# Performance work log

Measured on AMD Instinct MI355X. Metric: run time of the kernel, lower is better.

The kernel has to match this reference:

```python
import jax, jax.numpy as jnp
import numpy as np

# SelectiveAttention (keras) reference.
# - A single shared InputDense (D -> key_dim) projects query, key, value.
# - ComponentBuilder yields (filter_input=Q, context_input=banded K^T, _input=V):
#   scores = (Q K^T / sqrt(key_dim)) masked to the band |i-j| <= band_size
#   (the layer's Softmax sublayer is built but never invoked in call()).
# - attended = scores @ V, then OutputDense (key_dim -> D). Dropout inactive at inference.

def setup_inputs() -> dict:
    key = jax.random.key(0)
    ks = jax.random.split(key, 5)
    B, S, D, Dk = 4, 4096, 512, 64
    query = jax.random.normal(ks[0], (B, S, D), dtype=jnp.float32)
    value = jax.random.normal(ks[1], (B, S, D), dtype=jnp.float32)
    Wi = jax.random.normal(ks[2], (D, Dk), dtype=jnp.float32) * (1.0 / np.sqrt(D))
    bi = jnp.zeros((Dk,), dtype=jnp.float32)
    Wo = jax.random.normal(ks[3], (Dk, D), dtype=jnp.float32) * (1.0 / np.sqrt(Dk))
    bo = jnp.zeros((D,), dtype=jnp.float32)
    return {"query": query, "value": value, "Wi": Wi, "bi": bi,
            "Wo": Wo, "bo": bo, "band_size": 128}


def reference(query, value, Wi, bi, Wo, bo, band_size):
    Dk = Wi.shape[1]
    scale = 1.0 / jnp.sqrt(jnp.asarray(Dk, dtype=query.dtype))
    # shared input projection (same dense for q, k, v; key defaults to value)
    q = query @ Wi + bi            # [B,S,Dk]
    kv = value @ Wi + bi           # [B,S,Dk]  (k == v here)
    scores = jnp.einsum('bqd,bkd->bqk', q, kv) * scale  # [B,S,S]
    S = q.shape[1]
    idx = jnp.arange(S)
    band = (jnp.abs(idx[:, None] - idx[None, :]) <= band_size)  # [S,S] bool
    scores = jnp.where(band[None], scores, 0.0)
    attended = jnp.einsum('bqk,bkd->bqd', scores, kv)    # [B,S,Dk]
    return attended @ Wo + bo                            # [B,S,D]
```

## Files before the change

### kernel.cpp

```cpp
#include <hip/hip_runtime.h>
#include <math.h>


typedef __bf16 bf16;
using bf16x4  = __attribute__((ext_vector_type(4))) __bf16;
using bf16x8  = __attribute__((ext_vector_type(8))) __bf16;
using floatx4 = __attribute__((ext_vector_type(4))) float;

#define MFMA(a, b, c) __builtin_amdgcn_mfma_f32_16x16x32_bf16(a, b, c, 0, 0, 0)

__global__ __launch_bounds__(256) void prep_weights(
    const float* __restrict__ Wi, const float* __restrict__ Wo,
    bf16* __restrict__ WiT, bf16* __restrict__ WoT)
{
    __shared__ float T[64][65];
    const int blk = blockIdx.x, tid = threadIdx.x;
    if (blk < 8) {
        const int k0 = blk * 64;
        #pragma unroll
        for (int i = 0; i < 4; i++) {
            int idx4 = tid * 4 + i;
            int r = idx4 >> 4, c4 = (idx4 & 15) * 4;
            float4 f = *(const float4*)(Wi + (size_t)(k0 + r) * 64 + c4);
            T[r][c4 + 0] = f.x; T[r][c4 + 1] = f.y;
            T[r][c4 + 2] = f.z; T[r][c4 + 3] = f.w;
        }
        __syncthreads();
        #pragma unroll
        for (int i = 0; i < 2; i++) {
            int seg = tid * 2 + i;
            int n = seg >> 3, k8 = (seg & 7) * 8;
            bf16x8 v;
            #pragma unroll
            for (int j = 0; j < 8; j++) v[j] = (bf16)T[k8 + j][n];
            *(bf16x8*)(WiT + (size_t)n * 512 + k0 + k8) = v;
        }
    } else {
        const int n0 = (blk - 8) * 64;
        #pragma unroll
        for (int i = 0; i < 4; i++) {
            int idx4 = tid * 4 + i;
            int r = idx4 >> 4, c4 = (idx4 & 15) * 4;
            float4 f = *(const float4*)(Wo + (size_t)r * 512 + n0 + c4);
            T[r][c4 + 0] = f.x; T[r][c4 + 1] = f.y;
            T[r][c4 + 2] = f.z; T[r][c4 + 3] = f.w;
        }
        __syncthreads();
        #pragma unroll
        for (int i = 0; i < 2; i++) {
            int seg = tid * 2 + i;
            int n = seg >> 3, k8 = (seg & 7) * 8;
            bf16x8 v;
            #pragma unroll
            for (int j = 0; j < 8; j++) v[j] = (bf16)T[k8 + j][n];
            *(bf16x8*)(WoT + (size_t)(n0 + n) * 64 + k8) = v;
        }
    }
}

__global__ __launch_bounds__(256) void proj_in_kernel(
    const float* __restrict__ q, const float* __restrict__ v,
    const bf16* __restrict__ WiT, const float* __restrict__ bi,
    bf16* __restrict__ qp, bf16* __restrict__ kvp, bf16* __restrict__ kvT,
    int K, int S)
{
    const float* x = blockIdx.z ? v : q;
    bf16* y = blockIdx.z ? kvp : qp;
    __shared__ float P[4][16][68];
    const int tid = threadIdx.x;
    const int wave = tid >> 6, lane = tid & 63;
    const int lr = lane & 15, lq = lane >> 4;
    const int row0 = blockIdx.x * 16;
    const float* xrow = x + (size_t)(row0 + lr) * K + wave * 128;
    const bf16* wrow = WiT + wave * 128;

    floatx4 acc[4] = {};
    #pragma unroll
    for (int ks = 0; ks < 4; ks++) {
        const int k0 = ks * 32 + lq * 8;
        float4 a0 = *(const float4*)(xrow + k0);
        float4 a1 = *(const float4*)(xrow + k0 + 4);
        bf16x8 af;
        af[0] = (bf16)a0.x; af[1] = (bf16)a0.y; af[2] = (bf16)a0.z; af[3] = (bf16)a0.w;
        af[4] = (bf16)a1.x; af[5] = (bf16)a1.y; af[6] = (bf16)a1.z; af[7] = (bf16)a1.w;
        #pragma unroll
        for (int t = 0; t < 4; t++) {
            bf16x8 bfv = *(const bf16x8*)(wrow + (size_t)(t * 16 + lr) * K + k0);
            acc[t] = MFMA(af, bfv, acc[t]);
        }
    }
    #pragma unroll
    for (int t = 0; t < 4; t++)
        #pragma unroll
        for (int r = 0; r < 4; r++)
            P[wave][lq * 4 + r][t * 16 + lr] = acc[t][r];
    __syncthreads();

    {
        const int row = tid >> 4, c4 = (tid & 15) * 4;
        float4 s0 = *(const float4*)&P[0][row][c4];
        float4 s1 = *(const float4*)&P[1][row][c4];
        float4 s2 = *(const float4*)&P[2][row][c4];
        float4 s3 = *(const float4*)&P[3][row][c4];
        float4 bb = *(const float4*)(bi + c4);
        bf16x4 o;
        o[0] = (bf16)(s0.x + s1.x + s2.x + s3.x + bb.x);
        o[1] = (bf16)(s0.y + s1.y + s2.y + s3.y + bb.y);
        o[2] = (bf16)(s0.z + s1.z + s2.z + s3.z + bb.z);
        o[3] = (bf16)(s0.w + s1.w + s2.w + s3.w + bb.w);
        *(bf16x4*)(y + (size_t)(row0 + row) * 64 + c4) = o;
    }
    if (blockIdx.z) {
        const int d = tid >> 2, s4 = (tid & 3) * 4;
        const int b = row0 >> 12, s0r = row0 & (S - 1);
        const float bb = bi[d];
        bf16x4 o;
        #pragma unroll
        for (int i = 0; i < 4; i++) {
            float s = P[0][s4 + i][d] + P[1][s4 + i][d]
                    + P[2][s4 + i][d] + P[3][s4 + i][d] + bb;
            o[i] = (bf16)s;
        }
        *(bf16x4*)(kvT + ((size_t)b * 64 + d) * S + s0r + s4) = o;
    }
}

__global__ __launch_bounds__(256) void band_attn_out_kernel(
    const bf16* __restrict__ qp, const bf16* __restrict__ kvp,
    const bf16* __restrict__ kvT, const int* __restrict__ band_ptr,
    const bf16* __restrict__ WoT, const float* __restrict__ bo,
    float* __restrict__ out, int S, float scale)
{
    __shared__ bf16 Ss[4][2][16][88];
    const int tid = threadIdx.x;
    const int wave = tid >> 6, lane = tid & 63;
    const int lr = lane & 15, lq = lane >> 4;
    const int gw = blockIdx.x * 4 + wave;
    const int b = gw >> 8;
    const int q0 = (gw & 255) * 16;
    const int band = band_ptr[0];

    const bf16* qb = qp + ((size_t)b * S + q0) * 64;
    bf16x8 qf0 = *(const bf16x8*)(qb + lr * 64 + lq * 8);
    bf16x8 qf1 = *(const bf16x8*)(qb + lr * 64 + 32 + lq * 8);

    floatx4 acc[4] = {};
    const int ch_lo = (q0 - band) >> 6;
    #pragma unroll
    for (int cc = 0; cc < 5; cc++) {
        const int kj0 = (ch_lo + cc) * 64;
        bf16 (*strip)[88] = Ss[wave][cc & 1];
        floatx4 sc[4] = {};
        #pragma unroll
        for (int t = 0; t < 4; t++) {
            int kr = kj0 + t * 16 + lr;
            int krc = min(max(kr, 0), S - 1);
            const bf16* kp = kvp + ((size_t)b * S + krc) * 64;
            bf16x8 b0 = *(const bf16x8*)(kp + lq * 8);
            bf16x8 b1 = *(const bf16x8*)(kp + 32 + lq * 8);
            sc[t] = MFMA(qf0, b0, sc[t]);
            sc[t] = MFMA(qf1, b1, sc[t]);
        }
        #pragma unroll
        for (int t = 0; t < 4; t++) {
            int kj = kj0 + t * 16 + lr;
            bool kv_ok = (kj >= 0) && (kj < S);
            #pragma unroll
            for (int r = 0; r < 4; r++) {
                int qi = q0 + lq * 4 + r;
                int dlt = qi - kj; dlt = dlt < 0 ? -dlt : dlt;
                float vv = (kv_ok && dlt <= band) ? sc[t][r] * scale : 0.f;
                strip[lq * 4 + r][t * 16 + lr] = (bf16)vv;
            }
        }
        #pragma unroll
        for (int ks = 0; ks < 2; ks++) {
            bf16x8 sa = *(const bf16x8*)(&strip[lr][ks * 32 + lq * 8]);
            int kb = kj0 + ks * 32 + lq * 8;
            int kbc = min(max(kb, 0), S - 8);
            #pragma unroll
            for (int t = 0; t < 4; t++) {
                bf16x8 vb = *(const bf16x8*)(kvT + ((size_t)b * 64 + t * 16 + lr) * S + kbc);
                acc[t] = MFMA(sa, vb, acc[t]);
            }
        }
    }

    bf16 (*strip)[88] = Ss[wave][0];
    #pragma unroll
    for (int t = 0; t < 4; t++)
        #pragma unroll
        for (int r = 0; r < 4; r++)
            strip[lq * 4 + r][t * 16 + lr] = (bf16)acc[t][r];
    bf16x8 af0 = *(const bf16x8*)(&strip[lr][lq * 8]);
    bf16x8 af1 = *(const bf16x8*)(&strip[lr][32 + lq * 8]);
    float* orow = out + ((size_t)b * S + q0) * 512;
    #pragma unroll 8
    for (int tp = 0; tp < 32; tp++) {
        const bf16* wp = WoT + (size_t)(tp * 16 + lr) * 64;
        bf16x8 b0 = *(const bf16x8*)(wp + lq * 8);
        bf16x8 b1 = *(const bf16x8*)(wp + 32 + lq * 8);
        floatx4 o = {};
        o = MFMA(af0, b0, o);
        o = MFMA(af1, b1, o);
        float bb = bo[tp * 16 + lr];
        #pragma unroll
        for (int r = 0; r < 4; r++)
            orow[(size_t)(lq * 4 + r) * 512 + tp * 16 + lr] = o[r] + bb;
    }
}

extern "C" void kernel_launch(void* const* d_in, const int* in_sizes, int n_in,
                              void* d_out, int out_size, void* d_ws, size_t ws_size,
                              hipStream_t stream) {
    const float* query = (const float*)d_in[0];
    const float* value = (const float*)d_in[1];
    const float* Wi    = (const float*)d_in[2];
    const float* bi    = (const float*)d_in[3];
    const float* Wo    = (const float*)d_in[4];
    const float* bo    = (const float*)d_in[5];
    const int*   band  = (const int*)d_in[6];
    float* out = (float*)d_out;

    const int Dk = in_sizes[3];
    const int D  = in_sizes[5];
    const int S  = 4096;
    const int BS = in_sizes[0] / D;
    const int B  = BS / S;
    const float scale = 1.0f / sqrtf((float)Dk);

    bf16* WiT = (bf16*)d_ws;
    bf16* WoT = WiT + 32768;
    bf16* qp  = WoT + 32768;
    bf16* kvp = qp  + (size_t)BS * 64;
    bf16* kvT = kvp + (size_t)BS * 64;

    prep_weights<<<16, 256, 0, stream>>>(Wi, Wo, WiT, WoT);

    proj_in_kernel<<<dim3(BS / 16, 1, 2), 256, 0, stream>>>(
        query, value, WiT, bi, qp, kvp, kvT, D, S);

    band_attn_out_kernel<<<dim3(BS / 64), 256, 0, stream>>>(
        qp, kvp, kvT, band, WoT, bo, out, S, scale);
}
```

Measured before the change: 150.9 us.

## Split band chunks and output projection across waves per query tile

Each block now handles a single 16-row query tile instead of four. Its waves split the five key chunks (wave 0 takes two) and reduce partial results through shared memory. The output projection is then split across waves, eight column tiles each. The softmax scale is folded into the Q projection so the attention loop skips a multiply. This launches four times more blocks to raise parallelism, at the cost of extra shared-memory reduction, two barriers and load imbalance across waves.

```diff
diff --git a/kernel.cpp b/kernel.cpp
--- a/kernel.cpp
+++ b/kernel.cpp
@@ -62,10 +62,11 @@
     const float* __restrict__ q, const float* __restrict__ v,
     const bf16* __restrict__ WiT, const float* __restrict__ bi,
     bf16* __restrict__ qp, bf16* __restrict__ kvp, bf16* __restrict__ kvT,
-    int K, int S)
+    int K, int S, float scale)
 {
     const float* x = blockIdx.z ? v : q;
     bf16* y = blockIdx.z ? kvp : qp;
+    const float sc = blockIdx.z ? 1.0f : scale;
     __shared__ float P[4][16][68];
     const int tid = threadIdx.x;
     const int wave = tid >> 6, lane = tid & 63;
@@ -104,10 +105,10 @@
         float4 s3 = *(const float4*)&P[3][row][c4];
         float4 bb = *(const float4*)(bi + c4);
         bf16x4 o;
-        o[0] = (bf16)(s0.x + s1.x + s2.x + s3.x + bb.x);
-        o[1] = (bf16)(s0.y + s1.y + s2.y + s3.y + bb.y);
-        o[2] = (bf16)(s0.z + s1.z + s2.z + s3.z + bb.z);
-        o[3] = (bf16)(s0.w + s1.w + s2.w + s3.w + bb.w);
+        o[0] = (bf16)((s0.x + s1.x + s2.x + s3.x + bb.x) * sc);
+        o[1] = (bf16)((s0.y + s1.y + s2.y + s3.y + bb.y) * sc);
+        o[2] = (bf16)((s0.z + s1.z + s2.z + s3.z + bb.z) * sc);
+        o[3] = (bf16)((s0.w + s1.w + s2.w + s3.w + bb.w) * sc);
         *(bf16x4*)(y + (size_t)(row0 + row) * 64 + c4) = o;
     }
     if (blockIdx.z) {
@@ -129,15 +130,17 @@
     const bf16* __restrict__ qp, const bf16* __restrict__ kvp,
     const bf16* __restrict__ kvT, const int* __restrict__ band_ptr,
     const bf16* __restrict__ WoT, const float* __restrict__ bo,
-    float* __restrict__ out, int S, float scale)
+    float* __restrict__ out, int S)
 {
-    __shared__ bf16 Ss[4][2][16][88];
+    __shared__ bf16 Ss[4][16][88];
+    __shared__ float P[4][16][68];
+    __shared__ bf16 St[16][72];
     const int tid = threadIdx.x;
     const int wave = tid >> 6, lane = tid & 63;
     const int lr = lane & 15, lq = lane >> 4;
-    const int gw = blockIdx.x * 4 + wave;
-    const int b = gw >> 8;
-    const int q0 = (gw & 255) * 16;
+    const int gs = blockIdx.x;
+    const int b = gs >> 8;
+    const int q0 = (gs & 255) * 16;
     const int band = band_ptr[0];
 
     const bf16* qb = qp + ((size_t)b * S + q0) * 64;
@@ -147,56 +150,74 @@
     floatx4 acc[4] = {};
     const int ch_lo = (q0 - band) >> 6;
     #pragma unroll
-    for (int cc = 0; cc < 5; cc++) {
-        const int kj0 = (ch_lo + cc) * 64;
-        bf16 (*strip)[88] = Ss[wave][cc & 1];
-        floatx4 sc[4] = {};
-        #pragma unroll
-        for (int t = 0; t < 4; t++) {
-            int kr = kj0 + t * 16 + lr;
-            int krc = min(max(kr, 0), S - 1);
-            const bf16* kp = kvp + ((size_t)b * S + krc) * 64;
-            bf16x8 b0 = *(const bf16x8*)(kp + lq * 8);
-            bf16x8 b1 = *(const bf16x8*)(kp + 32 + lq * 8);
-            sc[t] = MFMA(qf0, b0, sc[t]);
-            sc[t] = MFMA(qf1, b1, sc[t]);
-        }
-        #pragma unroll
-        for (int t = 0; t < 4; t++) {
-            int kj = kj0 + t * 16 + lr;
-            bool kv_ok = (kj >= 0) && (kj < S);
-            #pragma unroll
-            for (int r = 0; r < 4; r++) {
-                int qi = q0 + lq * 4 + r;
-                int dlt = qi - kj; dlt = dlt < 0 ? -dlt : dlt;
-                float vv = (kv_ok && dlt <= band) ? sc[t][r] * scale : 0.f;
-                strip[lq * 4 + r][t * 16 + lr] = (bf16)vv;
+    for (int pass = 0; pass < 2; pass++) {
+        const int cc = wave + pass * 4;
+        if (cc <= 4) {
+            const int kj0 = (ch_lo + cc) * 64;
+            floatx4 sc[4] = {};
+            #pragma unroll
+            for (int t = 0; t < 4; t++) {
+                int kr = kj0 + t * 16 + lr;
+                int krc = min(max(kr, 0), S - 1);
+                const bf16* kp = kvp + ((size_t)b * S + krc) * 64;
+                bf16x8 b0 = *(const bf16x8*)(kp + lq * 8);
+                bf16x8 b1 = *(const bf16x8*)(kp + 32 + lq * 8);
+                sc[t] = MFMA(qf0, b0, sc[t]);
+                sc[t] = MFMA(qf1, b1, sc[t]);
             }
-        }
-        #pragma unroll
-        for (int ks = 0; ks < 2; ks++) {
-            bf16x8 sa = *(const bf16x8*)(&strip[lr][ks * 32 + lq * 8]);
-            int kb = kj0 + ks * 32 + lq * 8;
-            int kbc = min(max(kb, 0), S - 8);
             #pragma unroll
             for (int t = 0; t < 4; t++) {
-                bf16x8 vb = *(const bf16x8*)(kvT + ((size_t)b * 64 + t * 16 + lr) * S + kbc);
-                acc[t] = MFMA(sa, vb, acc[t]);
+                int kj = kj0 + t * 16 + lr;
+                bool kv_ok = (kj >= 0) && (kj < S);
+                #pragma unroll
+                for (int r = 0; r < 4; r++) {
+                    int qi = q0 + lq * 4 + r;
+                    int dlt = qi - kj; dlt = dlt < 0 ? -dlt : dlt;
+                    float vv = (kv_ok && dlt <= band) ? sc[t][r] : 0.f;
+                    Ss[wave][lq * 4 + r][t * 16 + lr] = (bf16)vv;
+                }
             }
-        }
-    }
-
-    bf16 (*strip)[88] = Ss[wave][0];
+            #pragma unroll
+            for (int ks = 0; ks < 2; ks++) {
+                bf16x8 sa = *(const bf16x8*)(&Ss[wave][lr][ks * 32 + lq * 8]);
+                int kb = kj0 + ks * 32 + lq * 8;
+                int kbc = min(max(kb, 0), S - 8);
+                #pragma unroll
+                for (int t = 0; t < 4; t++) {
+                    bf16x8 vb = *(const bf16x8*)(kvT + ((size_t)b * 64 + t * 16 + lr) * S + kbc);
+                    acc[t] = MFMA(sa, vb, acc[t]);
+                }
+            }
+        }
+    }
     #pragma unroll
     for (int t = 0; t < 4; t++)
         #pragma unroll
         for (int r = 0; r < 4; r++)
-            strip[lq * 4 + r][t * 16 + lr] = (bf16)acc[t][r];
-    bf16x8 af0 = *(const bf16x8*)(&strip[lr][lq * 8]);
-    bf16x8 af1 = *(const bf16x8*)(&strip[lr][32 + lq * 8]);
+            P[wave][lq * 4 + r][t * 16 + lr] = acc[t][r];
+    __syncthreads();
+
+    {
+        const int row = tid >> 4, c4 = (tid & 15) * 4;
+        float4 s0 = *(const float4*)&P[0][row][c4];
+        float4 s1 = *(const float4*)&P[1][row][c4];
+        float4 s2 = *(const float4*)&P[2][row][c4];
+        float4 s3 = *(const float4*)&P[3][row][c4];
+        bf16x4 o;
+        o[0] = (bf16)(s0.x + s1.x + s2.x + s3.x);
+        o[1] = (bf16)(s0.y + s1.y + s2.y + s3.y);
+        o[2] = (bf16)(s0.z + s1.z + s2.z + s3.z);
+        o[3] = (bf16)(s0.w + s1.w + s2.w + s3.w);
+        *(bf16x4*)(&St[row][c4]) = o;
+    }
+    __syncthreads();
+
+    bf16x8 af0 = *(const bf16x8*)(&St[lr][lq * 8]);
+    bf16x8 af1 = *(const bf16x8*)(&St[lr][32 + lq * 8]);
     float* orow = out + ((size_t)b * S + q0) * 512;
-    #pragma unroll 8
-    for (int tp = 0; tp < 32; tp++) {
+    #pragma unroll
+    for (int i = 0; i < 8; i++) {
+        const int tp = wave * 8 + i;
         const bf16* wp = WoT + (size_t)(tp * 16 + lr) * 64;
         bf16x8 b0 = *(const bf16x8*)(wp + lq * 8);
         bf16x8 b1 = *(const bf16x8*)(wp + 32 + lq * 8);
@@ -238,8 +259,8 @@
     prep_weights<<<16, 256, 0, stream>>>(Wi, Wo, WiT, WoT);
 
     proj_in_kernel<<<dim3(BS / 16, 1, 2), 256, 0, stream>>>(
-        query, value, WiT, bi, qp, kvp, kvT, D, S);
-
-    band_attn_out_kernel<<<dim3(BS / 64), 256, 0, stream>>>(
-        qp, kvp, kvT, band, WoT, bo, out, S, scale);
-}
+        query, value, WiT, bi, qp, kvp, kvT, D, S, scale);
+
+    band_attn_out_kernel<<<dim3(BS / 16), 256, 0, stream>>>(
+        qp, kvp, kvT, band, WoT, bo, out, S);
+}
```

Result: faster. 146.2 us (-3.1%).
